# Optimization experiments

Hardware: AMD Instinct MI355X
Metric: run time of the kernel (lower is better)

Reference implementation:

```python
import jax, jax.numpy as jnp
import numpy as np

N = 8192
F = 512
H = 256
O = 128
C = 64
E = 262144


def gcn_conv(x, W, b, src, dst, num_nodes):
    # PyG GCNConv: h = XW; add self-loops; symmetric deg^{-1/2} normalization; scatter-add; + bias
    h = x @ W  # [N, out]
    deg = jnp.zeros((num_nodes,), h.dtype).at[dst].add(1.0) + 1.0  # self-loop included
    dinv = jax.lax.rsqrt(deg)
    norm = (dinv[src] * dinv[dst])[:, None]  # [E, 1]
    agg = jnp.zeros_like(h).at[dst].add(h[src] * norm)
    agg = agg + h * (1.0 / deg)[:, None]  # self-loop contribution: deg^{-1/2} * deg^{-1/2}
    return agg + b


def setup_inputs() -> dict:
    key = jax.random.key(0)
    ks = jax.random.split(key, 12)
    x = jax.random.normal(ks[0], (N, F), jnp.float32)
    edge_index = jax.random.randint(ks[1], (2, E), 0, N, jnp.int64)
    eps = jax.random.normal(ks[2], (N, C), jnp.float32)
    s1 = 1.0 / np.sqrt(F)
    s2 = 1.0 / np.sqrt(H)
    s3 = 1.0 / np.sqrt(O)
    W1 = jax.random.uniform(ks[3], (F, H), jnp.float32, -s1, s1)
    b1 = jnp.zeros((H,), jnp.float32)
    W2 = jax.random.uniform(ks[4], (H, O), jnp.float32, -s2, s2)
    b2 = jnp.zeros((O,), jnp.float32)
    Wmu = jax.random.uniform(ks[5], (O, C), jnp.float32, -s3, s3)
    bmu = jax.random.uniform(ks[6], (C,), jnp.float32, -s3, s3)
    Wlv = jax.random.uniform(ks[7], (O, C), jnp.float32, -s3, s3)
    blv = jax.random.uniform(ks[8], (C,), jnp.float32, -s3, s3)
    return {"x": x, "edge_index": edge_index, "eps": eps,
            "W1": W1, "b1": b1, "W2": W2, "b2": b2,
            "Wmu": Wmu, "bmu": bmu, "Wlv": Wlv, "blv": blv}


def reference(x, edge_index, eps, W1, b1, W2, b2, Wmu, bmu, Wlv, blv):
    src, dst = edge_index[0], edge_index[1]
    n = x.shape[0]
    h = jax.nn.relu(gcn_conv(x, W1, b1, src, dst, n))
    z = gcn_conv(h, W2, b2, src, dst, n)  # [N, O]
    mu = z @ Wmu + bmu       # [N, C]
    logvar = z @ Wlv + blv   # [N, C]
    std = jnp.exp(0.5 * logvar)
    zr = mu + eps * std      # reparameterize
    adj_recon = jax.nn.sigmoid(zr @ zr.T)  # [N, N]
    return (adj_recon, mu, logvar)
```

## Files before the change

### kernel.cpp

```cpp
#include <hip/hip_runtime.h>
#include <hip/hip_bf16.h>

#define N_NODES 8192
#define F_IN    512
#define H_DIM   256
#define O_DIM   128
#define C_DIM   64
#define E_EDGES 262144
#define BCAP    96

typedef __attribute__((ext_vector_type(8))) short bf16x8;
typedef __attribute__((ext_vector_type(8))) _Float16 f16x8;
typedef __attribute__((ext_vector_type(4))) float f32x4;

__device__ inline unsigned short f2bf(float v) {
    __hip_bfloat16 h = __float2bfloat16(v);
    return *reinterpret_cast<unsigned short*>(&h);
}
__device__ inline float bf2f(unsigned short u) {
    return __uint_as_float((unsigned)u << 16);
}
__device__ inline void split2(float v, unsigned short& hi, unsigned short& lo) {
    hi = f2bf(v);
    lo = f2bf(v - bf2f(hi));
}
__device__ inline float4 bf4_to_f4(ushort4 u) {
    float4 f;
    f.x = bf2f(u.x); f.y = bf2f(u.y); f.z = bf2f(u.z); f.w = bf2f(u.w);
    return f;
}
__device__ inline bf16x8 pack_bf8(float4 a, float4 b) {
    bf16x8 r;
    r[0] = (short)f2bf(a.x); r[1] = (short)f2bf(a.y);
    r[2] = (short)f2bf(a.z); r[3] = (short)f2bf(a.w);
    r[4] = (short)f2bf(b.x); r[5] = (short)f2bf(b.y);
    r[6] = (short)f2bf(b.z); r[7] = (short)f2bf(b.w);
    return r;
}

__global__ __launch_bounds__(256) void prep_kernel(
    const float* __restrict__ W1, unsigned short* __restrict__ w1th, unsigned short* __restrict__ w1tl,
    const float* __restrict__ W2, unsigned short* __restrict__ w2th, unsigned short* __restrict__ w2tl,
    int* __restrict__ cnt)
{
    const int NW1 = F_IN * H_DIM;
    const int NW2 = H_DIM * O_DIM;
    int idx = blockIdx.x * 256 + threadIdx.x;
    if (idx < N_NODES) cnt[idx] = 0;
    if (idx < NW1) {
        int k = idx / H_DIM, n = idx % H_DIM;
        unsigned short h, l;
        split2(W1[idx], h, l);
        w1th[n * F_IN + k] = h;
        w1tl[n * F_IN + k] = l;
    } else if (idx < NW1 + NW2) {
        int j = idx - NW1;
        int k = j / O_DIM, n = j % O_DIM;
        unsigned short h, l;
        split2(W2[j], h, l);
        w2th[n * H_DIM + k] = h;
        w2tl[n * H_DIM + k] = l;
    }
}

__global__ __launch_bounds__(256) void gemm1_kernel(
    const float* __restrict__ x,
    const unsigned short* __restrict__ Bth, const unsigned short* __restrict__ Btl,
    const int* __restrict__ srcv, const int* __restrict__ dstv,
    int* __restrict__ cnt, int* __restrict__ slots,
    unsigned short* __restrict__ out)
{
    {
        int flat = (blockIdx.y * gridDim.x + blockIdx.x) * 256 + threadIdx.x;
        int e0 = flat * 4;
#pragma unroll
        for (int j = 0; j < 4; ++j) {
            int d = dstv[e0 + j];
            int pos = atomicAdd(&cnt[d], 1);
            slots[d * BCAP + pos] = srcv[e0 + j];
        }
    }

    constexpr int N = H_DIM, K = F_IN, MW = 2, NW = 4;
    const int tid = threadIdx.x;
    const int lane = tid & 63;
    const int wid = tid >> 6;
    const int r = lane & 15;
    const int kg = lane >> 4;
    const int m0 = blockIdx.y * (2 * MW * 16) + (wid >> 1) * (MW * 16);
    const int n0 = blockIdx.x * (2 * NW * 16) + (wid & 1) * (NW * 16);

    f32x4 acc[MW][NW];
#pragma unroll
    for (int mi = 0; mi < MW; ++mi)
#pragma unroll
        for (int ni = 0; ni < NW; ++ni) acc[mi][ni] = (f32x4){0.f, 0.f, 0.f, 0.f};

    for (int k0 = 0; k0 < K; k0 += 32) {
        const int kof = k0 + kg * 8;
        bf16x8 a[MW], bh[NW], bl[NW];
#pragma unroll
        for (int mi = 0; mi < MW; ++mi) {
            const float* xr = x + (size_t)(m0 + mi * 16 + r) * K + kof;
            float4 f0 = *(const float4*)xr;
            float4 f1 = *(const float4*)(xr + 4);
            a[mi] = pack_bf8(f0, f1);
        }
#pragma unroll
        for (int ni = 0; ni < NW; ++ni) {
            size_t off = (size_t)(n0 + ni * 16 + r) * K + kof;
            bh[ni] = *(const bf16x8*)(Bth + off);
            bl[ni] = *(const bf16x8*)(Btl + off);
        }
#pragma unroll
        for (int mi = 0; mi < MW; ++mi)
#pragma unroll
            for (int ni = 0; ni < NW; ++ni) {
                acc[mi][ni] = __builtin_amdgcn_mfma_f32_16x16x32_bf16(a[mi], bh[ni], acc[mi][ni], 0, 0, 0);
                acc[mi][ni] = __builtin_amdgcn_mfma_f32_16x16x32_bf16(a[mi], bl[ni], acc[mi][ni], 0, 0, 0);
            }
    }

#pragma unroll
    for (int mi = 0; mi < MW; ++mi) {
        int rowb = m0 + mi * 16 + kg * 4;
#pragma unroll
        for (int ni = 0; ni < NW; ++ni) {
            int col = n0 + ni * 16 + r;
#pragma unroll
            for (int i = 0; i < 4; ++i)
                out[(size_t)(rowb + i) * N + col] = f2bf(acc[mi][ni][i]);
        }
    }
}

__global__ __launch_bounds__(256) void gather_gemm2_kernel(
    const unsigned short* __restrict__ raw,
    const int* __restrict__ cnt, const int* __restrict__ slots,
    const float* __restrict__ b1,
    const unsigned short* __restrict__ w2th, const unsigned short* __restrict__ w2tl,
    unsigned short* __restrict__ g2b)
{
    __shared__ unsigned short hs[16 * 256];
    const int tid = threadIdx.x;
    const int wid = tid >> 6;
    const int lane = tid & 63;
    const int nb = blockIdx.x * 16;
    const ushort4* G4 = (const ushort4*)raw;

    for (int q = 0; q < 4; ++q) {
        const int ln = wid * 4 + q;
        const int node = nb + ln;
        const int deg = cnt[node];
        const int* sl = slots + node * BCAP;
        const float di = rsqrtf((float)deg + 1.0f);

        float4 selfv = bf4_to_f4(G4[(size_t)node * 64 + lane]);
        float4 acc, acc2;
        acc.x = di * selfv.x; acc.y = di * selfv.y;
        acc.z = di * selfv.z; acc.w = di * selfv.w;
        acc2 = make_float4(0.f, 0.f, 0.f, 0.f);

        int e = 0;
        for (; e + 8 <= deg; e += 8) {
            int s[8];
            ushort4 u[8];
            float d[8];
#pragma unroll
            for (int j = 0; j < 8; ++j) s[j] = sl[e + j];
#pragma unroll
            for (int j = 0; j < 8; ++j) u[j] = G4[(size_t)s[j] * 64 + lane];
#pragma unroll
            for (int j = 0; j < 8; ++j) d[j] = rsqrtf((float)cnt[s[j]] + 1.0f);
#pragma unroll
            for (int j = 0; j < 8; j += 2) {
                float4 v0 = bf4_to_f4(u[j]);
                float4 v1 = bf4_to_f4(u[j + 1]);
                acc.x = fmaf(d[j], v0.x, acc.x);     acc.y = fmaf(d[j], v0.y, acc.y);
                acc.z = fmaf(d[j], v0.z, acc.z);     acc.w = fmaf(d[j], v0.w, acc.w);
                acc2.x = fmaf(d[j+1], v1.x, acc2.x); acc2.y = fmaf(d[j+1], v1.y, acc2.y);
                acc2.z = fmaf(d[j+1], v1.z, acc2.z); acc2.w = fmaf(d[j+1], v1.w, acc2.w);
            }
        }
        for (; e < deg; ++e) {
            int s0 = sl[e];
            float d0 = rsqrtf((float)cnt[s0] + 1.0f);
            float4 v0 = bf4_to_f4(G4[(size_t)s0 * 64 + lane]);
            acc.x = fmaf(d0, v0.x, acc.x); acc.y = fmaf(d0, v0.y, acc.y);
            acc.z = fmaf(d0, v0.z, acc.z); acc.w = fmaf(d0, v0.w, acc.w);
        }
        acc.x += acc2.x; acc.y += acc2.y; acc.z += acc2.z; acc.w += acc2.w;

        const float4 bv = ((const float4*)b1)[lane];
        float4 rr;
        rr.x = di * acc.x + bv.x;
        rr.y = di * acc.y + bv.y;
        rr.z = di * acc.z + bv.z;
        rr.w = di * acc.w + bv.w;
        rr.x = rr.x > 0.f ? rr.x : 0.f;
        rr.y = rr.y > 0.f ? rr.y : 0.f;
        rr.z = rr.z > 0.f ? rr.z : 0.f;
        rr.w = rr.w > 0.f ? rr.w : 0.f;

        ushort4 hv;
        hv.x = f2bf(rr.x); hv.y = f2bf(rr.y); hv.z = f2bf(rr.z); hv.w = f2bf(rr.w);
        int s0 = (lane >> 1) ^ (ln & 7);
        *(ushort4*)((char*)hs + ln * 512 + (s0 << 4) + (lane & 1) * 8) = hv;
    }
    __syncthreads();

    const int r = lane & 15;
    const int kg = lane >> 4;
    const int wn = wid * 32;

    f32x4 acc[2];
    acc[0] = (f32x4){0.f, 0.f, 0.f, 0.f};
    acc[1] = (f32x4){0.f, 0.f, 0.f, 0.f};

    for (int k0 = 0; k0 < H_DIM; k0 += 32) {
        int slot = ((k0 >> 3) + kg) ^ (r & 7);
        bf16x8 a = *(const bf16x8*)((const char*)hs + r * 512 + (slot << 4));
#pragma unroll
        for (int ni = 0; ni < 2; ++ni) {
            size_t off = (size_t)(wn + ni * 16 + r) * H_DIM + k0 + kg * 8;
            bf16x8 bh = *(const bf16x8*)(w2th + off);
            bf16x8 bl = *(const bf16x8*)(w2tl + off);
            acc[ni] = __builtin_amdgcn_mfma_f32_16x16x32_bf16(a, bh, acc[ni], 0, 0, 0);
            acc[ni] = __builtin_amdgcn_mfma_f32_16x16x32_bf16(a, bl, acc[ni], 0, 0, 0);
        }
    }

    float di4[4];
#pragma unroll
    for (int i = 0; i < 4; ++i) di4[i] = rsqrtf((float)cnt[nb + kg * 4 + i] + 1.0f);
#pragma unroll
    for (int ni = 0; ni < 2; ++ni) {
#pragma unroll
        for (int i = 0; i < 4; ++i) {
            int row = nb + kg * 4 + i;
            g2b[(size_t)row * O_DIM + wn + ni * 16 + r] = f2bf(di4[i] * acc[ni][i]);
        }
    }
}

__global__ __launch_bounds__(128) void gather_head_kernel(
    const unsigned short* __restrict__ g2,
    const int* __restrict__ cnt, const int* __restrict__ slots,
    const float* __restrict__ b2,
    const float* __restrict__ Wmu, const float* __restrict__ bmu,
    const float* __restrict__ Wlv, const float* __restrict__ blv,
    const float* __restrict__ eps,
    float* __restrict__ mu_out, float* __restrict__ lv_out,
    _Float16* __restrict__ zr)
{
    __shared__ float zsw[2][O_DIM];
    __shared__ float zs[O_DIM];
    __shared__ float mu_s[C_DIM];
    __shared__ float lv_s[C_DIM];
    const int node = blockIdx.x;
    const int t = threadIdx.x;
    const int w = t >> 6;
    const int lane = t & 63;

    const int deg = cnt[node];
    const int* sl = slots + node * BCAP;
    const unsigned int* G2 = (const unsigned int*)g2;

    float a0 = 0.f, a1 = 0.f, c0 = 0.f, c1 = 0.f;
    if (w == 0) {
        unsigned int u = G2[(size_t)node * 64 + lane];
        a0 = bf2f((unsigned short)u);
        a1 = bf2f((unsigned short)(u >> 16));
    }
    int e = w;
    for (; e + 6 < deg; e += 8) {
        unsigned int u0 = G2[(size_t)sl[e]     * 64 + lane];
        unsigned int u1 = G2[(size_t)sl[e + 2] * 64 + lane];
        unsigned int u2 = G2[(size_t)sl[e + 4] * 64 + lane];
        unsigned int u3 = G2[(size_t)sl[e + 6] * 64 + lane];
        a0 += bf2f((unsigned short)u0) + bf2f((unsigned short)u1);
        a1 += bf2f((unsigned short)(u0 >> 16)) + bf2f((unsigned short)(u1 >> 16));
        c0 += bf2f((unsigned short)u2) + bf2f((unsigned short)u3);
        c1 += bf2f((unsigned short)(u2 >> 16)) + bf2f((unsigned short)(u3 >> 16));
    }
    for (; e < deg; e += 2) {
        unsigned int u = G2[(size_t)sl[e] * 64 + lane];
        a0 += bf2f((unsigned short)u);
        a1 += bf2f((unsigned short)(u >> 16));
    }
    zsw[w][2 * lane]     = a0 + c0;
    zsw[w][2 * lane + 1] = a1 + c1;
    __syncthreads();

    float dv = rsqrtf((float)deg + 1.0f);
    zs[t] = dv * (zsw[0][t] + zsw[1][t]) + b2[t];
    __syncthreads();

    const int c = t & 63;
    const float* W = (t < 64) ? Wmu : Wlv;
    float s = 0.f;
#pragma unroll 8
    for (int k = 0; k < O_DIM; ++k) s += zs[k] * W[k * C_DIM + c];
    if (t < 64) {
        s += bmu[c];
        mu_out[(size_t)node * C_DIM + c] = s;
        mu_s[c] = s;
    } else {
        s += blv[c];
        lv_out[(size_t)node * C_DIM + c] = s;
        lv_s[c] = s;
    }
    __syncthreads();
    if (t < 64) {
        float stdv = __expf(0.5f * lv_s[c]);
        float v = mu_s[c] + eps[(size_t)node * C_DIM + c] * stdv;
        zr[(size_t)node * C_DIM + c] = (_Float16)v;
    }
}

__global__ __launch_bounds__(256) void adj_mfma_kernel(
    const _Float16* __restrict__ Z, float* __restrict__ out)
{
    const int tid = threadIdx.x;
    const int lane = tid & 63;
    const int wid = tid >> 6;
    const int r = lane & 15;
    const int kg = lane >> 4;
    const int m0 = blockIdx.y * 128 + (wid >> 1) * 64;
    const int n0 = blockIdx.x * 128 + (wid & 1) * 64;

    f16x8 a[4][2], b[4][2];
#pragma unroll
    for (int mi = 0; mi < 4; ++mi)
#pragma unroll
        for (int ks = 0; ks < 2; ++ks) {
            a[mi][ks] = *(const f16x8*)(Z + (size_t)(m0 + mi * 16 + r) * C_DIM + ks * 32 + kg * 8);
            b[mi][ks] = *(const f16x8*)(Z + (size_t)(n0 + mi * 16 + r) * C_DIM + ks * 32 + kg * 8);
        }

    f32x4 acc[4][4];
#pragma unroll
    for (int mi = 0; mi < 4; ++mi)
#pragma unroll
        for (int ni = 0; ni < 4; ++ni) acc[mi][ni] = (f32x4){0.f, 0.f, 0.f, 0.f};

#pragma unroll
    for (int mi = 0; mi < 4; ++mi)
#pragma unroll
        for (int ni = 0; ni < 4; ++ni) {
            acc[mi][ni] = __builtin_amdgcn_mfma_f32_16x16x32_f16(a[mi][0], b[ni][0], acc[mi][ni], 0, 0, 0);
            acc[mi][ni] = __builtin_amdgcn_mfma_f32_16x16x32_f16(a[mi][1], b[ni][1], acc[mi][ni], 0, 0, 0);
        }

#pragma unroll
    for (int mi = 0; mi < 4; ++mi) {
        int rowb = m0 + mi * 16 + kg * 4;
#pragma unroll
        for (int ni = 0; ni < 4; ++ni) {
            int col = n0 + ni * 16 + r;
#pragma unroll
            for (int i = 0; i < 4; ++i) {
                float v = acc[mi][ni][i];
                float e = __expf(-v);
                float sg = __builtin_amdgcn_rcpf(1.0f + e);
                __builtin_nontemporal_store(sg, &out[(size_t)(rowb + i) * N_NODES + col]);
            }
        }
    }
}

extern "C" void kernel_launch(void* const* d_in, const int* in_sizes, int n_in,
                              void* d_out, int out_size, void* d_ws, size_t ws_size,
                              hipStream_t stream) {
    const float* x   = (const float*)d_in[0];
    const int*   ei  = (const int*)  d_in[1];
    const float* eps = (const float*)d_in[2];
    const float* W1  = (const float*)d_in[3];
    const float* b1  = (const float*)d_in[4];
    const float* W2  = (const float*)d_in[5];
    const float* b2  = (const float*)d_in[6];
    const float* Wmu = (const float*)d_in[7];
    const float* bmu = (const float*)d_in[8];
    const float* Wlv = (const float*)d_in[9];
    const float* blv = (const float*)d_in[10];
    float* out = (float*)d_out;

    const int* srcv = ei;
    const int* dstv = ei + E_EDGES;

    char* p = (char*)d_ws;
    auto carve = [&](size_t bytes) -> void* {
        void* q = (void*)p;
        p += (bytes + 255) & ~(size_t)255;
        return q;
    };
    int* cnt      = (int*)carve(N_NODES * 4);
    int* slots    = (int*)carve((size_t)N_NODES * BCAP * 4);
    unsigned short* w1th = (unsigned short*)carve((size_t)F_IN * H_DIM * 2);
    unsigned short* w1tl = (unsigned short*)carve((size_t)F_IN * H_DIM * 2);
    unsigned short* w2th = (unsigned short*)carve((size_t)H_DIM * O_DIM * 2);
    unsigned short* w2tl = (unsigned short*)carve((size_t)H_DIM * O_DIM * 2);
    unsigned short* raw1 = (unsigned short*)carve((size_t)N_NODES * H_DIM * 2);
    unsigned short* g2b  = (unsigned short*)carve((size_t)N_NODES * O_DIM * 2);
    _Float16* zr         = (_Float16*)carve((size_t)N_NODES * C_DIM * 2);

    float* mu_out = out + (size_t)N_NODES * N_NODES;
    float* lv_out = mu_out + (size_t)N_NODES * C_DIM;

    {
        const int total = F_IN * H_DIM + H_DIM * O_DIM;
        prep_kernel<<<(total + 255) / 256, 256, 0, stream>>>(
            W1, w1th, w1tl, W2, w2th, w2tl, cnt);
    }

    {
        dim3 grid(H_DIM / 128, N_NODES / 64);
        gemm1_kernel<<<grid, 256, 0, stream>>>(
            x, w1th, w1tl, srcv, dstv, cnt, slots, raw1);
    }

    gather_gemm2_kernel<<<N_NODES / 16, 256, 0, stream>>>(
        raw1, cnt, slots, b1, w2th, w2tl, g2b);

    gather_head_kernel<<<N_NODES, 128, 0, stream>>>(
        g2b, cnt, slots, b2, Wmu, bmu, Wlv, blv, eps,
        mu_out, lv_out, zr);

    {
        dim3 grid(N_NODES / 128, N_NODES / 128);
        adj_mfma_kernel<<<grid, 256, 0, stream>>>(zr, out);
    }
}
```

Measured before the change: 179.8 us.

## Drop split-bf16 for W1, pre-convert x to bf16, shrink gemm1 tiles

The first GEMM now uses a single bf16 copy of W1 instead of a hi/lo split, which halves its MFMA count and its W1 loads. x is converted to bf16 once in the prep kernel, so gemm1 loads bf16 directly instead of converting fp32 per tile. The gemm1 tile narrows to 64 columns, doubling the grid, and each thread bins two edges instead of four. This loses some accuracy in the first layer, and the extra pass writing xb adds about 8 MB of traffic.

Result: faster. 173.7 us (-3.4%).

```diff
diff --git a/kernel.cpp b/kernel.cpp
--- a/kernel.cpp
+++ b/kernel.cpp
@@ -29,32 +29,29 @@
     f.x = bf2f(u.x); f.y = bf2f(u.y); f.z = bf2f(u.z); f.w = bf2f(u.w);
     return f;
 }
-__device__ inline bf16x8 pack_bf8(float4 a, float4 b) {
-    bf16x8 r;
-    r[0] = (short)f2bf(a.x); r[1] = (short)f2bf(a.y);
-    r[2] = (short)f2bf(a.z); r[3] = (short)f2bf(a.w);
-    r[4] = (short)f2bf(b.x); r[5] = (short)f2bf(b.y);
-    r[6] = (short)f2bf(b.z); r[7] = (short)f2bf(b.w);
-    return r;
-}
 
 __global__ __launch_bounds__(256) void prep_kernel(
-    const float* __restrict__ W1, unsigned short* __restrict__ w1th, unsigned short* __restrict__ w1tl,
+    const float* __restrict__ x, unsigned short* __restrict__ xb,
+    const float* __restrict__ W1, unsigned short* __restrict__ w1t,
     const float* __restrict__ W2, unsigned short* __restrict__ w2th, unsigned short* __restrict__ w2tl,
     int* __restrict__ cnt)
 {
+    const int NX4 = N_NODES * F_IN / 4;
     const int NW1 = F_IN * H_DIM;
     const int NW2 = H_DIM * O_DIM;
     int idx = blockIdx.x * 256 + threadIdx.x;
     if (idx < N_NODES) cnt[idx] = 0;
-    if (idx < NW1) {
-        int k = idx / H_DIM, n = idx % H_DIM;
-        unsigned short h, l;
-        split2(W1[idx], h, l);
-        w1th[n * F_IN + k] = h;
-        w1tl[n * F_IN + k] = l;
-    } else if (idx < NW1 + NW2) {
-        int j = idx - NW1;
+    if (idx < NX4) {
+        float4 v = ((const float4*)x)[idx];
+        ushort4 b;
+        b.x = f2bf(v.x); b.y = f2bf(v.y); b.z = f2bf(v.z); b.w = f2bf(v.w);
+        ((ushort4*)xb)[idx] = b;
+    } else if (idx < NX4 + NW1) {
+        int j = idx - NX4;
+        int k = j / H_DIM, n = j % H_DIM;
+        w1t[n * F_IN + k] = f2bf(W1[j]);
+    } else if (idx < NX4 + NW1 + NW2) {
+        int j = idx - NX4 - NW1;
         int k = j / O_DIM, n = j % O_DIM;
         unsigned short h, l;
         split2(W2[j], h, l);
@@ -64,24 +61,24 @@
 }
 
 __global__ __launch_bounds__(256) void gemm1_kernel(
-    const float* __restrict__ x,
-    const unsigned short* __restrict__ Bth, const unsigned short* __restrict__ Btl,
+    const unsigned short* __restrict__ xb,
+    const unsigned short* __restrict__ Bt,
     const int* __restrict__ srcv, const int* __restrict__ dstv,
     int* __restrict__ cnt, int* __restrict__ slots,
     unsigned short* __restrict__ out)
 {
     {
         int flat = (blockIdx.y * gridDim.x + blockIdx.x) * 256 + threadIdx.x;
-        int e0 = flat * 4;
-#pragma unroll
-        for (int j = 0; j < 4; ++j) {
+        int e0 = flat * 2;
+#pragma unroll
+        for (int j = 0; j < 2; ++j) {
             int d = dstv[e0 + j];
             int pos = atomicAdd(&cnt[d], 1);
             slots[d * BCAP + pos] = srcv[e0 + j];
         }
     }
 
-    constexpr int N = H_DIM, K = F_IN, MW = 2, NW = 4;
+    constexpr int N = H_DIM, K = F_IN, MW = 2, NW = 2;
     const int tid = threadIdx.x;
     const int lane = tid & 63;
     const int wid = tid >> 6;
@@ -98,27 +95,18 @@
 
     for (int k0 = 0; k0 < K; k0 += 32) {
         const int kof = k0 + kg * 8;
-        bf16x8 a[MW], bh[NW], bl[NW];
-#pragma unroll
-        for (int mi = 0; mi < MW; ++mi) {
-            const float* xr = x + (size_t)(m0 + mi * 16 + r) * K + kof;
-            float4 f0 = *(const float4*)xr;
-            float4 f1 = *(const float4*)(xr + 4);
-            a[mi] = pack_bf8(f0, f1);
-        }
-#pragma unroll
-        for (int ni = 0; ni < NW; ++ni) {
-            size_t off = (size_t)(n0 + ni * 16 + r) * K + kof;
-            bh[ni] = *(const bf16x8*)(Bth + off);
-            bl[ni] = *(const bf16x8*)(Btl + off);
-        }
+        bf16x8 a[MW], b[NW];
 #pragma unroll
         for (int mi = 0; mi < MW; ++mi)
-#pragma unroll
-            for (int ni = 0; ni < NW; ++ni) {
-                acc[mi][ni] = __builtin_amdgcn_mfma_f32_16x16x32_bf16(a[mi], bh[ni], acc[mi][ni], 0, 0, 0);
-                acc[mi][ni] = __builtin_amdgcn_mfma_f32_16x16x32_bf16(a[mi], bl[ni], acc[mi][ni], 0, 0, 0);
-            }
+            a[mi] = *(const bf16x8*)(xb + (size_t)(m0 + mi * 16 + r) * K + kof);
+#pragma unroll
+        for (int ni = 0; ni < NW; ++ni)
+            b[ni] = *(const bf16x8*)(Bt + (size_t)(n0 + ni * 16 + r) * K + kof);
+#pragma unroll
+        for (int mi = 0; mi < MW; ++mi)
+#pragma unroll
+            for (int ni = 0; ni < NW; ++ni)
+                acc[mi][ni] = __builtin_amdgcn_mfma_f32_16x16x32_bf16(a[mi], b[ni], acc[mi][ni], 0, 0, 0);
     }
 
 #pragma unroll
@@ -396,8 +384,8 @@
     };
     int* cnt      = (int*)carve(N_NODES * 4);
     int* slots    = (int*)carve((size_t)N_NODES * BCAP * 4);
-    unsigned short* w1th = (unsigned short*)carve((size_t)F_IN * H_DIM * 2);
-    unsigned short* w1tl = (unsigned short*)carve((size_t)F_IN * H_DIM * 2);
+    unsigned short* xb   = (unsigned short*)carve((size_t)N_NODES * F_IN * 2);
+    unsigned short* w1t  = (unsigned short*)carve((size_t)F_IN * H_DIM * 2);
     unsigned short* w2th = (unsigned short*)carve((size_t)H_DIM * O_DIM * 2);
     unsigned short* w2tl = (unsigned short*)carve((size_t)H_DIM * O_DIM * 2);
     unsigned short* raw1 = (unsigned short*)carve((size_t)N_NODES * H_DIM * 2);
@@ -408,15 +396,15 @@
     float* lv_out = mu_out + (size_t)N_NODES * C_DIM;
 
     {
-        const int total = F_IN * H_DIM + H_DIM * O_DIM;
+        const int total = N_NODES * F_IN / 4 + F_IN * H_DIM + H_DIM * O_DIM;
         prep_kernel<<<(total + 255) / 256, 256, 0, stream>>>(
-            W1, w1th, w1tl, W2, w2th, w2tl, cnt);
+            x, xb, W1, w1t, W2, w2th, w2tl, cnt);
     }
 
     {
-        dim3 grid(H_DIM / 128, N_NODES / 64);
+        dim3 grid(H_DIM / 64, N_NODES / 64);
         gemm1_kernel<<<grid, 256, 0, stream>>>(
-            x, w1th, w1tl, srcv, dstv, cnt, slots, raw1);
+            xb, w1t, srcv, dstv, cnt, slots, raw1);
     }
 
     gather_gemm2_kernel<<<N_NODES / 16, 256, 0, stream>>>(
```
